# Performance work log

Measured on AMD Instinct MI355X. Metric: run time of the kernel, lower is better.

Reference implementation:

```python
import jax, jax.numpy as jnp
import numpy as np

MAX_LANES = 5
DELTA_V = 1.0
DELTA_D = 6.0


def setup_inputs() -> dict:
    key = jax.random.key(0)
    k1, k2 = jax.random.split(key)
    targets = jax.random.randint(k1, (32, 360, 640), 0, 6, dtype=jnp.int32)
    embedding_vector = jax.random.normal(k2, (32, 4, 360, 640), dtype=jnp.float32)
    return {"targets": targets, "embedding_vector": embedding_vector}


def reference(targets, embedding_vector):
    B, C, H, W = embedding_vector.shape
    L = MAX_LANES
    P = H * W
    t = targets.reshape(B, P)                      # [B,P] labels 0..L
    e = embedding_vector.reshape(B, C, P)          # [B,C,P]

    # per-(batch, lane) segment counts and means
    onehot = (t[:, None, :] == jnp.arange(1, L + 1, dtype=t.dtype)[None, :, None])  # [B,L,P]
    counts = onehot.sum(-1)                        # [B,L] int
    valid = counts > 1                             # lane used only if >1 points
    sums = jnp.einsum('blp,bcp->blc', onehot.astype(e.dtype), e)   # [B,L,C]
    means = sums / jnp.maximum(counts, 1)[..., None].astype(e.dtype)  # [B,L,C]

    # ---- variance (pull) loss: per-point distance to its lane mean ----
    means_ext = jnp.concatenate([jnp.zeros((B, 1, C), e.dtype), means], axis=1)  # [B,L+1,C]
    mean_pix = jnp.take_along_axis(means_ext, t[..., None].astype(jnp.int32), axis=1)  # [B,P,C]
    diff = e.transpose(0, 2, 1) - mean_pix         # [B,P,C]
    sq = jnp.sum(diff * diff, axis=-1)             # [B,P]
    dist = jnp.sqrt(jnp.maximum(sq, 1e-12))
    valid_ext = jnp.concatenate([jnp.zeros((B, 1), bool), valid], axis=1)  # [B,L+1]
    pix_valid = jnp.take_along_axis(valid_ext, t.astype(jnp.int32), axis=1)  # [B,P]
    hinge = jax.nn.relu(dist - DELTA_V)
    dist_sum = jnp.sum(jnp.where(pix_valid, hinge * hinge, 0.0))
    point_count = jnp.sum(jnp.where(valid, counts, 0)).astype(e.dtype)
    dist_loss = jnp.where(point_count > 0, dist_sum / jnp.maximum(point_count, 1.0), 0.0)

    # ---- distance (push) loss: pdist over valid lane means per batch ----
    d = means[:, :, None, :] - means[:, None, :, :]          # [B,L,L,C]
    psq = jnp.sum(d * d, axis=-1)                            # [B,L,L]
    pd = jnp.sqrt(jnp.maximum(psq, 1e-12))
    iu = jnp.arange(L)
    pair_mask = valid[:, :, None] & valid[:, None, :] & (iu[:, None] < iu[None, :])  # [B,L,L]
    ph = jax.nn.relu(DELTA_D - pd)
    per_batch_sum = jnp.sum(jnp.where(pair_mask, ph * ph, 0.0), axis=(1, 2))  # [B]
    npairs = pair_mask.sum((1, 2)).astype(e.dtype)           # [B]
    batch_has = npairs > 0                                   # needs >=2 valid lanes
    var_b = jnp.where(batch_has, per_batch_sum / jnp.maximum(npairs, 1.0), 0.0)
    n_batches = batch_has.sum().astype(e.dtype)
    var_loss = jnp.where(n_batches > 0, var_b.sum() / jnp.maximum(n_batches, 1.0), 0.0)

    return dist_loss + var_loss
```

## Files before the change

### kernel.cpp

```cpp
#include <hip/hip_runtime.h>
#include <math.h>

#define B 32
#define C 4
#define P (360*640)
#define L 5
#define DELTA_V 1.0f
#define DELTA_D 6.0f

#define BLKX 45
#define ITER1 5
#define G4 (P/4)
#define NBLK3 (B*BLKX)

__device__ __forceinline__ float waveReduce(float v) {
#pragma unroll
    for (int off = 32; off; off >>= 1) v += __shfl_down(v, off, 64);
    return v;
}

__global__ __launch_bounds__(256, 4) void seg_sums_k(const int* __restrict__ tgt,
                                                     const float* __restrict__ emb,
                                                     float* __restrict__ sums,
                                                     float* __restrict__ cnts) {
    const int x = blockIdx.x, c = blockIdx.y, b = blockIdx.z;
    const int tid = threadIdx.x;

    const int4*   t4 = (const int4*)(tgt + (size_t)b * P);
    const float4* ec = (const float4*)(emb + ((size_t)b * C + c) * P);

    int4   tv[ITER1];
    float4 ev[ITER1];
#pragma unroll
    for (int it = 0; it < ITER1; ++it) {
        const int g = (x + it * BLKX) * 256 + tid;
        tv[it] = t4[g];
        ev[it] = ec[g];
    }

    float s[L], n[L];
#pragma unroll
    for (int l = 0; l < L; ++l) { s[l] = 0.f; n[l] = 0.f; }

    auto acc1 = [&](int tt, float e) {
#pragma unroll
        for (int l = 0; l < L; ++l) {
            float m = (tt == l + 1) ? 1.0f : 0.0f;
            n[l] += m;
            s[l] = fmaf(m, e, s[l]);
        }
    };
#pragma unroll
    for (int it = 0; it < ITER1; ++it) {
        acc1(tv[it].x, ev[it].x);
        acc1(tv[it].y, ev[it].y);
        acc1(tv[it].z, ev[it].z);
        acc1(tv[it].w, ev[it].w);
    }

    float vals[2*L];
#pragma unroll
    for (int l = 0; l < L; ++l) { vals[l] = s[l]; vals[L + l] = n[l]; }

    __shared__ float red[4][2*L];
    const int lane = tid & 63, wave = tid >> 6;
#pragma unroll
    for (int k = 0; k < 2*L; ++k) {
        float r = waveReduce(vals[k]);
        if (lane == 0) red[wave][k] = r;
    }
    __syncthreads();
    if (tid < L) {
        float r = red[0][tid] + red[1][tid] + red[2][tid] + red[3][tid];
        sums[((size_t)(b * BLKX + x) * C + c) * L + tid] = r;
    } else if (c == 0 && tid < 2*L) {
        float r = red[0][tid] + red[1][tid] + red[2][tid] + red[3][tid];
        cnts[(size_t)(b * BLKX + x) * L + (tid - L)] = r;
    }
}

__global__ __launch_bounds__(256) void means_k(const float* __restrict__ sums,
                                               const float* __restrict__ cnts,
                                               float* __restrict__ means,
                                               float* __restrict__ validf,
                                               float* __restrict__ cntv) {
    const int seg  = (blockIdx.x * 256 + threadIdx.x) >> 6;
    const int lane = threadIdx.x & 63;
    if (seg >= B * L) return;
    const int b = seg / L, l = seg % L;

    float v0=0.f, v1=0.f, v2=0.f, v3=0.f, vc=0.f;
    if (lane < BLKX) {
        const size_t base = (size_t)(b * BLKX + lane) * C * L;
        v0 = sums[base + 0*L + l];
        v1 = sums[base + 1*L + l];
        v2 = sums[base + 2*L + l];
        v3 = sums[base + 3*L + l];
        vc = cnts[(size_t)(b * BLKX + lane) * L + l];
    }
    v0 = waveReduce(v0); v1 = waveReduce(v1); v2 = waveReduce(v2);
    v3 = waveReduce(v3); vc = waveReduce(vc);
    if (lane == 0) {
        const float inv = 1.0f / fmaxf(vc, 1.0f);
        const bool  v   = vc > 1.5f;
        means[seg*4+0] = v0 * inv;
        means[seg*4+1] = v1 * inv;
        means[seg*4+2] = v2 * inv;
        means[seg*4+3] = v3 * inv;
        validf[seg] = v ? 1.f : 0.f;
        cntv[seg]   = v ? vc  : 0.f;
    }
}

__global__ __launch_bounds__(256, 4) void pull_k(const int* __restrict__ tgt,
                                                 const float* __restrict__ emb,
                                                 const float* __restrict__ means,
                                                 const float* __restrict__ validf,
                                                 float* __restrict__ part3) {
    __shared__ float4 lmean[L + 1];
    __shared__ float  lvalid[L + 1];
    __shared__ float  lred[4];
    const int x = blockIdx.x, b = blockIdx.y;
    const int tid = threadIdx.x;

    if (tid == 0) { lmean[0] = make_float4(0.f, 0.f, 0.f, 0.f); lvalid[0] = 0.f; }
    else if (tid <= L) {
        lmean[tid]  = *(const float4*)(means + ((size_t)b*L + (tid-1)) * 4);
        lvalid[tid] = validf[b*L + (tid-1)];
    }
    __syncthreads();

    const int4*   t4 = (const int4*)(tgt + (size_t)b * P);
    const float4* e0 = (const float4*)(emb + ((size_t)b*C + 0) * P);
    const float4* e1 = (const float4*)(emb + ((size_t)b*C + 1) * P);
    const float4* e2 = (const float4*)(emb + ((size_t)b*C + 2) * P);
    const float4* e3 = (const float4*)(emb + ((size_t)b*C + 3) * P);

    float acc = 0.f;
    auto proc1 = [&](int tt, float v0, float v1, float v2, float v3) {
        float4 m = lmean[tt];
        float d0 = v0 - m.x, d1 = v1 - m.y, d2 = v2 - m.z, d3 = v3 - m.w;
        float sq   = d0*d0 + d1*d1 + d2*d2 + d3*d3;
        float dist = sqrtf(fmaxf(sq, 1e-12f));
        float h    = fmaxf(dist - DELTA_V, 0.f);
        acc = fmaf(lvalid[tt] * h, h, acc);
    };

    int g = x * 256 + tid;
    int4   ta = t4[g];
    float4 p0 = e0[g], p1 = e1[g], p2 = e2[g], p3 = e3[g];
#pragma unroll
    for (int it = 0; it < ITER1 - 1; ++it) {
        const int gn = (x + (it + 1) * BLKX) * 256 + tid;
        int4   tb = t4[gn];
        float4 q0 = e0[gn], q1 = e1[gn], q2 = e2[gn], q3 = e3[gn];
        proc1(ta.x, p0.x, p1.x, p2.x, p3.x);
        proc1(ta.y, p0.y, p1.y, p2.y, p3.y);
        proc1(ta.z, p0.z, p1.z, p2.z, p3.z);
        proc1(ta.w, p0.w, p1.w, p2.w, p3.w);
        ta = tb; p0 = q0; p1 = q1; p2 = q2; p3 = q3;
    }
    proc1(ta.x, p0.x, p1.x, p2.x, p3.x);
    proc1(ta.y, p0.y, p1.y, p2.y, p3.y);
    proc1(ta.z, p0.z, p1.z, p2.z, p3.z);
    proc1(ta.w, p0.w, p1.w, p2.w, p3.w);

    float r = waveReduce(acc);
    const int lane = tid & 63, wave = tid >> 6;
    if (lane == 0) lred[wave] = r;
    __syncthreads();
    if (tid == 0)
        part3[b * BLKX + x] = lred[0] + lred[1] + lred[2] + lred[3];
}

__global__ __launch_bounds__(256) void finish_k(const float* __restrict__ part3,
                                                const float* __restrict__ means,
                                                const float* __restrict__ validf,
                                                const float* __restrict__ cntv,
                                                float* __restrict__ out) {
    __shared__ float red[4][4];
    const int tid = threadIdx.x;
    const int lane = tid & 63, wave = tid >> 6;

    float vb = 0.f, has = 0.f;
    if (tid < B) {
        const float* mb = means  + tid * L * 4;
        const float* vv = validf + tid * L;
        float ssum = 0.f, np = 0.f;
#pragma unroll
        for (int i = 0; i < L; ++i)
#pragma unroll
            for (int j = i + 1; j < L; ++j) {
                float ok = vv[i] * vv[j];
                float d0 = mb[i*4+0] - mb[j*4+0];
                float d1 = mb[i*4+1] - mb[j*4+1];
                float d2 = mb[i*4+2] - mb[j*4+2];
                float d3 = mb[i*4+3] - mb[j*4+3];
                float psq = d0*d0 + d1*d1 + d2*d2 + d3*d3;
                float pd  = sqrtf(fmaxf(psq, 1e-12f));
                float ph  = fmaxf(DELTA_D - pd, 0.f);
                ssum += ok * ph * ph;
                np   += ok;
            }
        if (np > 0.f) { vb = ssum / np; has = 1.f; }
    }
    float pc = (tid < B*L) ? cntv[tid] : 0.f;
    float ps = 0.f;
    for (int i = tid; i < NBLK3; i += 256) ps += part3[i];

    float rvb = waveReduce(vb);
    float rhs = waveReduce(has);
    float rpc = waveReduce(pc);
    float rps = waveReduce(ps);
    if (lane == 0) { red[wave][0]=rvb; red[wave][1]=rhs; red[wave][2]=rpc; red[wave][3]=rps; }
    __syncthreads();
    if (tid == 0) {
        float svb = red[0][0]+red[1][0]+red[2][0]+red[3][0];
        float shs = red[0][1]+red[1][1]+red[2][1]+red[3][1];
        float spc = red[0][2]+red[1][2]+red[2][2]+red[3][2];
        float sps = red[0][3]+red[1][3]+red[2][3]+red[3][3];
        float var = (shs > 0.f) ? svb / shs : 0.f;
        float dl  = (spc > 0.f) ? sps / fmaxf(spc, 1.f) : 0.f;
        out[0] = dl + var;
    }
}

extern "C" void kernel_launch(void* const* d_in, const int* in_sizes, int n_in,
                              void* d_out, int out_size, void* d_ws, size_t ws_size,
                              hipStream_t stream) {
    const int*   tgt = (const int*)d_in[0];
    const float* emb = (const float*)d_in[1];

    float* ws     = (float*)d_ws;
    float* sums   = ws;
    float* cnts   = sums + (size_t)B*BLKX*C*L;
    float* means  = cnts + (size_t)B*BLKX*L;
    float* validf = means + B*L*4;
    float* cntv   = validf + B*L;
    float* part3  = cntv + B*L;

    seg_sums_k<<<dim3(BLKX, C, B), 256, 0, stream>>>(tgt, emb, sums, cnts);
    means_k<<<(B*L + 3) / 4, 256, 0, stream>>>(sums, cnts, means, validf, cntv);
    pull_k<<<dim3(BLKX, B), 256, 0, stream>>>(tgt, emb, means, validf, part3);
    finish_k<<<1, 256, 0, stream>>>(part3, means, validf, cntv, (float*)d_out);
}
```

Baseline: 218.6 us.

## Fuse means reduction into pull kernel and process two channels per sums block

```diff
diff --git a/kernel.cpp b/kernel.cpp
--- a/kernel.cpp
+++ b/kernel.cpp
@@ -10,8 +10,8 @@
 
 #define BLKX 45
 #define ITER1 5
-#define G4 (P/4)
 #define NBLK3 (B*BLKX)
+#define PSTRIDE 48
 
 __device__ __forceinline__ float waveReduce(float v) {
 #pragma unroll
@@ -21,120 +21,113 @@
 
 __global__ __launch_bounds__(256, 4) void seg_sums_k(const int* __restrict__ tgt,
                                                      const float* __restrict__ emb,
-                                                     float* __restrict__ sums,
-                                                     float* __restrict__ cnts) {
-    const int x = blockIdx.x, c = blockIdx.y, b = blockIdx.z;
+                                                     float* __restrict__ partial) {
+    const int xb = blockIdx.x, cp = blockIdx.y, b = blockIdx.z;
     const int tid = threadIdx.x;
-
-    const int4*   t4 = (const int4*)(tgt + (size_t)b * P);
-    const float4* ec = (const float4*)(emb + ((size_t)b * C + c) * P);
-
-    int4   tv[ITER1];
-    float4 ev[ITER1];
-#pragma unroll
-    for (int it = 0; it < ITER1; ++it) {
-        const int g = (x + it * BLKX) * 256 + tid;
-        tv[it] = t4[g];
-        ev[it] = ec[g];
-    }
-
-    float s[L], n[L];
-#pragma unroll
-    for (int l = 0; l < L; ++l) { s[l] = 0.f; n[l] = 0.f; }
-
-    auto acc1 = [&](int tt, float e) {
+    const int c0 = 2 * cp;
+
+    const int4*   t4  = (const int4*)(tgt + (size_t)b * P);
+    const float4* ea  = (const float4*)(emb + ((size_t)b * C + c0    ) * P);
+    const float4* eb  = (const float4*)(emb + ((size_t)b * C + c0 + 1) * P);
+
+    float s0[L], s1[L], n[L];
+#pragma unroll
+    for (int l = 0; l < L; ++l) { s0[l] = 0.f; s1[l] = 0.f; n[l] = 0.f; }
+
+    auto acc1 = [&](int tt, float x0, float x1) {
 #pragma unroll
         for (int l = 0; l < L; ++l) {
             float m = (tt == l + 1) ? 1.0f : 0.0f;
-            n[l] += m;
-            s[l] = fmaf(m, e, s[l]);
+            n[l]  += m;
+            s0[l]  = fmaf(m, x0, s0[l]);
+            s1[l]  = fmaf(m, x1, s1[l]);
         }
     };
-#pragma unroll
-    for (int it = 0; it < ITER1; ++it) {
-        acc1(tv[it].x, ev[it].x);
-        acc1(tv[it].y, ev[it].y);
-        acc1(tv[it].z, ev[it].z);
-        acc1(tv[it].w, ev[it].w);
-    }
-
-    float vals[2*L];
-#pragma unroll
-    for (int l = 0; l < L; ++l) { vals[l] = s[l]; vals[L + l] = n[l]; }
-
-    __shared__ float red[4][2*L];
+    auto consume = [&](const int4& tv, const float4& va, const float4& vb) {
+        acc1(tv.x, va.x, vb.x);
+        acc1(tv.y, va.y, vb.y);
+        acc1(tv.z, va.z, vb.z);
+        acc1(tv.w, va.w, vb.w);
+    };
+
+    int g = xb * 256 + tid;
+    int4   ta = t4[g];
+    float4 pa = ea[g], pb = eb[g];
+#pragma unroll
+    for (int it = 0; it < ITER1 - 1; ++it) {
+        const int gn = (xb + (it + 1) * BLKX) * 256 + tid;
+        int4   tb = t4[gn];
+        float4 qa = ea[gn], qb = eb[gn];
+        consume(ta, pa, pb);
+        ta = tb; pa = qa; pb = qb;
+    }
+    consume(ta, pa, pb);
+
+    float vals[15];
+#pragma unroll
+    for (int l = 0; l < L; ++l) { vals[l] = s0[l]; vals[L + l] = s1[l]; vals[10 + l] = n[l]; }
+
+    __shared__ float red[4][15];
     const int lane = tid & 63, wave = tid >> 6;
 #pragma unroll
-    for (int k = 0; k < 2*L; ++k) {
+    for (int k = 0; k < 15; ++k) {
         float r = waveReduce(vals[k]);
         if (lane == 0) red[wave][k] = r;
     }
     __syncthreads();
-    if (tid < L) {
-        float r = red[0][tid] + red[1][tid] + red[2][tid] + red[3][tid];
-        sums[((size_t)(b * BLKX + x) * C + c) * L + tid] = r;
-    } else if (c == 0 && tid < 2*L) {
-        float r = red[0][tid] + red[1][tid] + red[2][tid] + red[3][tid];
-        cnts[(size_t)(b * BLKX + x) * L + (tid - L)] = r;
-    }
-}
-
-__global__ __launch_bounds__(256) void means_k(const float* __restrict__ sums,
-                                               const float* __restrict__ cnts,
-                                               float* __restrict__ means,
-                                               float* __restrict__ validf,
-                                               float* __restrict__ cntv) {
-    const int seg  = (blockIdx.x * 256 + threadIdx.x) >> 6;
-    const int lane = threadIdx.x & 63;
-    if (seg >= B * L) return;
-    const int b = seg / L, l = seg % L;
-
-    float v0=0.f, v1=0.f, v2=0.f, v3=0.f, vc=0.f;
-    if (lane < BLKX) {
-        const size_t base = (size_t)(b * BLKX + lane) * C * L;
-        v0 = sums[base + 0*L + l];
-        v1 = sums[base + 1*L + l];
-        v2 = sums[base + 2*L + l];
-        v3 = sums[base + 3*L + l];
-        vc = cnts[(size_t)(b * BLKX + lane) * L + l];
-    }
-    v0 = waveReduce(v0); v1 = waveReduce(v1); v2 = waveReduce(v2);
-    v3 = waveReduce(v3); vc = waveReduce(vc);
-    if (lane == 0) {
-        const float inv = 1.0f / fmaxf(vc, 1.0f);
-        const bool  v   = vc > 1.5f;
-        means[seg*4+0] = v0 * inv;
-        means[seg*4+1] = v1 * inv;
-        means[seg*4+2] = v2 * inv;
-        means[seg*4+3] = v3 * inv;
-        validf[seg] = v ? 1.f : 0.f;
-        cntv[seg]   = v ? vc  : 0.f;
+    if (tid < 15) {
+        const float r = red[0][tid] + red[1][tid] + red[2][tid] + red[3][tid];
+        int v;
+        if (cp == 0) v = (tid < 10) ? tid : (tid + 10);
+        else         v = (tid < 10) ? (10 + tid) : -1;
+        if (v >= 0)
+            partial[((size_t)b * 25 + v) * PSTRIDE + xb] = r;
     }
 }
 
 __global__ __launch_bounds__(256, 4) void pull_k(const int* __restrict__ tgt,
                                                  const float* __restrict__ emb,
-                                                 const float* __restrict__ means,
-                                                 const float* __restrict__ validf,
-                                                 float* __restrict__ part3) {
+                                                 const float* __restrict__ partial,
+                                                 float* __restrict__ meansG,
+                                                 float* __restrict__ validG,
+                                                 float* __restrict__ cntvG,
+                                                 float* __restrict__ pullp) {
+    __shared__ float  praw[25];
     __shared__ float4 lmean[L + 1];
     __shared__ float  lvalid[L + 1];
     __shared__ float  lred[4];
-    const int x = blockIdx.x, b = blockIdx.y;
+    const int xb = blockIdx.x, b = blockIdx.y;
     const int tid = threadIdx.x;
-
-    if (tid == 0) { lmean[0] = make_float4(0.f, 0.f, 0.f, 0.f); lvalid[0] = 0.f; }
-    else if (tid <= L) {
-        lmean[tid]  = *(const float4*)(means + ((size_t)b*L + (tid-1)) * 4);
-        lvalid[tid] = validf[b*L + (tid-1)];
-    }
+    const int lane = tid & 63, wave = tid >> 6;
+
+    for (int v = wave; v < 25; v += 4) {
+        float pv = (lane < BLKX) ? partial[((size_t)b * 25 + v) * PSTRIDE + lane] : 0.f;
+        pv = waveReduce(pv);
+        if (lane == 0) praw[v] = pv;
+    }
+    __syncthreads();
+    if (tid < L) {
+        const float cnt = praw[20 + tid];
+        const bool  vld = cnt > 1.5f;
+        const float inv = 1.0f / fmaxf(cnt, 1.0f);
+        float4 m = make_float4(praw[tid] * inv, praw[5 + tid] * inv,
+                               praw[10 + tid] * inv, praw[15 + tid] * inv);
+        lmean[tid + 1]  = m;
+        lvalid[tid + 1] = vld ? 1.f : 0.f;
+        if (xb == 0) {
+            *(float4*)(meansG + ((size_t)b * L + tid) * 4) = m;
+            validG[b * L + tid] = vld ? 1.f : 0.f;
+            cntvG[b * L + tid]  = vld ? cnt : 0.f;
+        }
+    }
+    if (tid == 8) { lmean[0] = make_float4(0.f, 0.f, 0.f, 0.f); lvalid[0] = 0.f; }
     __syncthreads();
 
     const int4*   t4 = (const int4*)(tgt + (size_t)b * P);
-    const float4* e0 = (const float4*)(emb + ((size_t)b*C + 0) * P);
-    const float4* e1 = (const float4*)(emb + ((size_t)b*C + 1) * P);
-    const float4* e2 = (const float4*)(emb + ((size_t)b*C + 2) * P);
-    const float4* e3 = (const float4*)(emb + ((size_t)b*C + 3) * P);
+    const float4* e0 = (const float4*)(emb + ((size_t)b * C + 0) * P);
+    const float4* e1 = (const float4*)(emb + ((size_t)b * C + 1) * P);
+    const float4* e2 = (const float4*)(emb + ((size_t)b * C + 2) * P);
+    const float4* e3 = (const float4*)(emb + ((size_t)b * C + 3) * P);
 
     float acc = 0.f;
     auto proc1 = [&](int tt, float v0, float v1, float v2, float v3) {
@@ -146,12 +139,12 @@
         acc = fmaf(lvalid[tt] * h, h, acc);
     };
 
-    int g = x * 256 + tid;
+    int g = xb * 256 + tid;
     int4   ta = t4[g];
     float4 p0 = e0[g], p1 = e1[g], p2 = e2[g], p3 = e3[g];
 #pragma unroll
     for (int it = 0; it < ITER1 - 1; ++it) {
-        const int gn = (x + (it + 1) * BLKX) * 256 + tid;
+        const int gn = (xb + (it + 1) * BLKX) * 256 + tid;
         int4   tb = t4[gn];
         float4 q0 = e0[gn], q1 = e1[gn], q2 = e2[gn], q3 = e3[gn];
         proc1(ta.x, p0.x, p1.x, p2.x, p3.x);
@@ -166,17 +159,16 @@
     proc1(ta.w, p0.w, p1.w, p2.w, p3.w);
 
     float r = waveReduce(acc);
-    const int lane = tid & 63, wave = tid >> 6;
     if (lane == 0) lred[wave] = r;
     __syncthreads();
     if (tid == 0)
-        part3[b * BLKX + x] = lred[0] + lred[1] + lred[2] + lred[3];
-}
-
-__global__ __launch_bounds__(256) void finish_k(const float* __restrict__ part3,
-                                                const float* __restrict__ means,
-                                                const float* __restrict__ validf,
-                                                const float* __restrict__ cntv,
+        pullp[b * BLKX + xb] = lred[0] + lred[1] + lred[2] + lred[3];
+}
+
+__global__ __launch_bounds__(256) void finish_k(const float* __restrict__ pullp,
+                                                const float* __restrict__ meansG,
+                                                const float* __restrict__ validG,
+                                                const float* __restrict__ cntvG,
                                                 float* __restrict__ out) {
     __shared__ float red[4][4];
     const int tid = threadIdx.x;
@@ -184,8 +176,8 @@
 
     float vb = 0.f, has = 0.f;
     if (tid < B) {
-        const float* mb = means  + tid * L * 4;
-        const float* vv = validf + tid * L;
+        const float* mb = meansG + tid * L * 4;
+        const float* vv = validG + tid * L;
         float ssum = 0.f, np = 0.f;
 #pragma unroll
         for (int i = 0; i < L; ++i)
@@ -204,9 +196,9 @@
             }
         if (np > 0.f) { vb = ssum / np; has = 1.f; }
     }
-    float pc = (tid < B*L) ? cntv[tid] : 0.f;
+    float pc = (tid < B*L) ? cntvG[tid] : 0.f;
     float ps = 0.f;
-    for (int i = tid; i < NBLK3; i += 256) ps += part3[i];
+    for (int i = tid; i < NBLK3; i += 256) ps += pullp[i];
 
     float rvb = waveReduce(vb);
     float rhs = waveReduce(has);
@@ -231,16 +223,15 @@
     const int*   tgt = (const int*)d_in[0];
     const float* emb = (const float*)d_in[1];
 
-    float* ws     = (float*)d_ws;
-    float* sums   = ws;
-    float* cnts   = sums + (size_t)B*BLKX*C*L;
-    float* means  = cnts + (size_t)B*BLKX*L;
-    float* validf = means + B*L*4;
-    float* cntv   = validf + B*L;
-    float* part3  = cntv + B*L;
-
-    seg_sums_k<<<dim3(BLKX, C, B), 256, 0, stream>>>(tgt, emb, sums, cnts);
-    means_k<<<(B*L + 3) / 4, 256, 0, stream>>>(sums, cnts, means, validf, cntv);
-    pull_k<<<dim3(BLKX, B), 256, 0, stream>>>(tgt, emb, means, validf, part3);
-    finish_k<<<1, 256, 0, stream>>>(part3, means, validf, cntv, (float*)d_out);
-}
+    float* ws      = (float*)d_ws;
+    float* partial = ws;
+    float* meansG  = partial + (size_t)B*25*PSTRIDE;
+    float* validG  = meansG + (size_t)B*L*4;
+    float* cntvG   = validG + B*L;
+    float* pullp   = cntvG + B*L;
+
+    seg_sums_k<<<dim3(BLKX, 2, B), 256, 0, stream>>>(tgt, emb, partial);
+    pull_k<<<dim3(BLKX, B), 256, 0, stream>>>(tgt, emb, partial,
+                                              meansG, validG, cntvG, pullp);
+    finish_k<<<1, 256, 0, stream>>>(pullp, meansG, validG, cntvG, (float*)d_out);
+}
```

Measured after the change: 257.2 us. +17.7%, slower.
